# Kernel optimization log

Measured on AMD Instinct MI355X. Metric: run time of the kernel, lower is better.

## Reference

```python
import jax, jax.numpy as jnp
import numpy as np

T, B, D, H = 512, 64, 256, 512


def setup_inputs() -> dict:
    key = jax.random.key(0)
    k1, k2, k3, k4 = jax.random.split(key, 4)
    x = jax.random.normal(k1, (T, B, D), dtype=jnp.float32)
    should_reset = jax.random.randint(k2, (T, B), 0, 2, dtype=jnp.int32)
    # Linear([x, h]) -> 4H gates, Haiku/PyTorch-style fan-in init scale
    scale = 1.0 / np.sqrt(D + H)
    W = jax.random.normal(k3, (D + H, 4 * H), dtype=jnp.float32) * scale
    b = jax.random.normal(k4, (4 * H,), dtype=jnp.float32) * scale
    return {"x": x, "should_reset": should_reset, "W": W, "b": b}


def reference(x, should_reset, W, b):
    """ResetLSTM forward (reverse=False). x:[T,B,D], should_reset:[T,B] -> [T,B,H]."""
    h0 = jnp.zeros((x.shape[1], H), dtype=x.dtype)
    c0 = jnp.zeros((x.shape[1], H), dtype=x.dtype)
    reset = should_reset.astype(x.dtype)[..., None]  # [T,B,1]

    def step(carry, inp):
        h, c = carry
        xt, rt = inp
        keep = 1.0 - rt
        h = h * keep
        c = c * keep
        gates = jnp.concatenate([xt, h], axis=-1) @ W + b  # [B,4H]
        i, g, f, o = jnp.split(gates, 4, axis=-1)
        f = jax.nn.sigmoid(f + 1.0)  # Haiku forget bias +1
        i = jax.nn.sigmoid(i)
        g = jnp.tanh(g)
        o = jax.nn.sigmoid(o)
        new_c = f * c + i * g
        new_h = o * jnp.tanh(new_c)
        return (new_h, new_c), new_h

    _, outputs = jax.lax.scan(step, (h0, c0), (x, reset))
    return outputs  # [T,B,H]
```

## Files before the change

### kernel.cpp

```cpp
#include <hip/hip_runtime.h>

#define TSTEPS 512
#define BATCH  64
#define DIN    256
#define HID    512
#define NCH    8
#define VR     512
#define NRB    16
#define NUB    32
#define NWG    512
#define NTHR   256
#define HSST   520
#define GST    67

typedef __attribute__((ext_vector_type(8))) _Float16 f16x8;
typedef __attribute__((ext_vector_type(4))) _Float16 f16x4;
typedef __attribute__((ext_vector_type(4))) float f32x4;
typedef __attribute__((ext_vector_type(2))) float f32x2;

#define MFMA16(A,B,C) __builtin_amdgcn_mfma_f32_16x16x32_f16(A,B,C,0,0,0)
#define ALDU32(p) __hip_atomic_load(const_cast<unsigned*>(p), __ATOMIC_RELAXED, __HIP_MEMORY_SCOPE_AGENT)
#define ASTU32(p,v) __hip_atomic_store((p), (v), __ATOMIC_RELAXED, __HIP_MEMORY_SCOPE_AGENT)

__device__ __forceinline__ float sigm(float x) { return 1.0f / (1.0f + __expf(-x)); }

__device__ __forceinline__ void gld16_cc(f16x8& d, const void* p) {
  asm volatile("global_load_dwordx4 %0, %1, off sc0 sc1" : "=v"(d) : "v"(p));
}
__device__ __forceinline__ void gld16_l2(f16x8& d, const void* p) {
  asm volatile("global_load_dwordx4 %0, %1, off sc0" : "=v"(d) : "v"(p));
}
__device__ __forceinline__ void gld16_pin(f16x8& d, const void* p) {
  asm volatile("global_load_dwordx4 %0, %1, off" : "=v"(d) : "v"(p));
}

__global__ void conv_x(const float* __restrict__ x, _Float16* __restrict__ xh, int n4) {
  int i = blockIdx.x * 256 + threadIdx.x;
  if (i >= n4) return;
  float4 v = reinterpret_cast<const float4*>(x)[i];
  f16x4 o;
  o[0] = (_Float16)v.x; o[1] = (_Float16)v.y; o[2] = (_Float16)v.z; o[3] = (_Float16)v.w;
  *reinterpret_cast<f16x4*>(xh + (size_t)i * 4) = o;
}

__global__ void w_prep(const float* __restrict__ W,
                       _Float16* __restrict__ WxT, _Float16* __restrict__ WhT) {
  int idx = blockIdx.x * 256 + threadIdx.x;
  if (idx < NUB * 64 * 256) {
    int k = idx & 255, cc = (idx >> 8) & 63, ub = idx >> 14;
    int unit = cc >> 2, g = cc & 3;
    int gcol = g * HID + ub * 16 + unit;
    WxT[idx] = (_Float16)W[k * 2048 + gcol];
  } else if (idx < NUB * 64 * 256 + NUB * 64 * 512) {
    int j = idx - NUB * 64 * 256;
    int k = j & 511, cc = (j >> 9) & 63, ub = j >> 15;
    int unit = cc >> 2, g = cc & 3;
    int gcol = g * HID + ub * 16 + unit;
    WhT[j] = (_Float16)W[(DIN + k) * 2048 + gcol];
  }
}

__global__ void seg_prep(const int* __restrict__ rst, int* __restrict__ tS,
                         int* __restrict__ segLen, int* __restrict__ maxLenB) {
  __shared__ int sMax[NRB];
  const int b = threadIdx.x;
  if (b < NRB) sMax[b] = 0;
  __syncthreads();
  int lo = (TSTEPS + NCH - 1) / NCH, hi = TSTEPS;
  while (lo < hi) {
    int L = (lo + hi) >> 1;
    int pos = 0; bool ok = false;
    for (int s = 0; s < NCH; ++s) {
      int target = pos + L;
      if (target >= TSTEPS) { ok = true; break; }
      int t = target;
      while (t > pos && rst[t * BATCH + b] == 0) --t;
      if (t == pos) break;
      pos = t;
    }
    if (ok) hi = L; else lo = L + 1;
  }
  const int L = lo;
  int pos = 0;
  for (int c = 0; c < NCH; ++c) {
    int start = pos, end = pos;
    if (pos < TSTEPS) {
      int target = pos + L;
      if (target >= TSTEPS) end = TSTEPS;
      else { int t = target; while (t > pos && rst[t * BATCH + b] == 0) --t; end = t; }
      pos = end;
    }
    int vr = c * 64 + b;
    tS[vr] = start;
    segLen[vr] = end - start;
    atomicMax(&sMax[c * 2 + (b >> 5)], end - start);
  }
  __syncthreads();
  if (b < NRB) maxLenB[b] = sMax[b];
}

__global__ void __launch_bounds__(NTHR, 2)
lstm_persistent(const _Float16* __restrict__ xh,
                const int* __restrict__ rst,
                const float* __restrict__ bias,
                float* __restrict__ out,
                unsigned long long* __restrict__ hb,
                unsigned* __restrict__ flags,
                unsigned* __restrict__ xccb,
                const _Float16* __restrict__ WxT,
                const _Float16* __restrict__ WhT,
                const int* __restrict__ tS,
                const int* __restrict__ segLen,
                const int* __restrict__ maxLenB) {
  __shared__ _Float16 hS[32 * HSST];
  __shared__ float gateS[32 * GST];
  __shared__ float biasS[64];
  __shared__ int uniformS;

  const int tid = threadIdx.x, wg = blockIdx.x;
  const int ub = wg >> 4;
  const int rb = ((wg & 7) << 1) | ((wg >> 3) & 1);
  const int wgbase = wg & 15;
  const int vr0 = rb * 32;
  const int lane = tid & 63, wave = tid >> 6;
  const int colA = lane & 15, klo = (lane >> 4) * 8;

  unsigned myxcc;
  asm volatile("s_getreg_b32 %0, hwreg(HW_REG_XCC_ID)" : "=s"(myxcc));
  if (tid == 0) {
    uniformS = 1;
    ASTU32(xccb + wg * 16, 0x100u | (myxcc & 0xffu));
  }
  __syncthreads();
  if (tid < NUB) {
    int mwg = (tid << 4) | wgbase;
    unsigned v;
    do { v = ALDU32(xccb + mwg * 16); if (!v) __builtin_amdgcn_s_sleep(1); } while (!v);
    if ((v & 0xffu) != (myxcc & 0xffu)) uniformS = 0;
  }

  f16x8 wx[8], wh[16];
  {
    const _Float16* px = WxT + ((size_t)ub * 64 + wave * 16 + colA) * 256 + klo;
    const _Float16* ph = WhT + ((size_t)ub * 64 + wave * 16 + colA) * 512 + klo;
#pragma unroll
    for (int ch = 0; ch < 8; ++ch) gld16_pin(wx[ch], px + ch * 32);
#pragma unroll
    for (int ch = 0; ch < 16; ++ch) gld16_pin(wh[ch], ph + ch * 32);
    asm volatile("s_waitcnt vmcnt(0)" ::: "memory");
    __builtin_amdgcn_sched_barrier(0);
  }
  if (tid < 64) {
    int unit = tid >> 2, g = tid & 3;
    biasS[tid] = bias[g * HID + ub * 16 + unit];
  }

  int tSr0 = tS[vr0 + colA];
  int tSr1 = tS[vr0 + 16 + colA];

  const int crow = tid & 31, p = tid >> 5;
  const int vrc = vr0 + crow, bc = vrc & 63;
  const int tSc_ = tS[vrc], lenc_ = segLen[vrc];
  const int ML = maxLenB[rb];
  float cA = 0.f, cB = 0.f;

  __syncthreads();
  const bool useL2 = (uniformS != 0);
  float bA[4], bB[4];
#pragma unroll
  for (int g = 0; g < 4; ++g) { bA[g] = biasS[8 * p + g]; bB[g] = biasS[8 * p + 4 + g]; }

  const int srow = tid >> 3, ss = tid & 7;

  for (int k = 0; k < ML; ++k) {
    f32x4 acc0 = {0.f, 0.f, 0.f, 0.f}, acc1 = {0.f, 0.f, 0.f, 0.f};
    {
      int t0 = tSr0 + k; if (t0 > TSTEPS - 1) t0 = TSTEPS - 1;
      int t1 = tSr1 + k; if (t1 > TSTEPS - 1) t1 = TSTEPS - 1;
      const int b0 = (vr0 + colA) & 63, b1 = (vr0 + 16 + colA) & 63;
      const _Float16* x0 = xh + ((size_t)t0 * BATCH + b0) * DIN + klo;
      const _Float16* x1 = xh + ((size_t)t1 * BATCH + b1) * DIN + klo;
#pragma unroll
      for (int ch = 0; ch < 8; ++ch) {
        f16x8 a0 = *(const f16x8*)(x0 + ch * 32);
        f16x8 a1 = *(const f16x8*)(x1 + ch * 32);
        acc0 = MFMA16(a0, wx[ch], acc0);
        acc1 = MFMA16(a1, wx[ch], acc1);
      }
    }

    if (k) {
      if (tid < NUB) {
        const unsigned tgt = (unsigned)k;
        while (ALDU32(flags + ((tid << 4) | wgbase) * 16) < tgt)
          __builtin_amdgcn_s_sleep(1);
      }
      __syncthreads();
      asm volatile("" ::: "memory");

      {
        const char* hbase = (const char*)hb
            + (((size_t)(k & 1) * (VR * 128) + (size_t)(vr0 + srow) * 128) << 3)
            + ss * 16;
        f16x8 hq[8];
        if (useL2) {
#pragma unroll
          for (int j = 0; j < 8; ++j) gld16_l2(hq[j], hbase + j * 128);
        } else {
#pragma unroll
          for (int j = 0; j < 8; ++j) gld16_cc(hq[j], hbase + j * 128);
        }
        asm volatile("s_waitcnt vmcnt(0)" ::: "memory");
        __builtin_amdgcn_sched_barrier(0);
#pragma unroll
        for (int j = 0; j < 8; ++j)
          *(f16x8*)&hS[srow * HSST + ss * 8 + j * 64] = hq[j];
      }
      __syncthreads();

#pragma unroll
      for (int ch = 0; ch < 16; ++ch) {
        f16x8 a0 = *(const f16x8*)&hS[colA * HSST + ch * 32 + klo];
        f16x8 a1 = *(const f16x8*)&hS[(16 + colA) * HSST + ch * 32 + klo];
        acc0 = MFMA16(a0, wh[ch], acc0);
        acc1 = MFMA16(a1, wh[ch], acc1);
      }
    }

#pragma unroll
    for (int rr = 0; rr < 4; ++rr) {
      int row0 = (lane >> 4) * 4 + rr;
      gateS[row0 * GST + wave * 16 + colA]        = acc0[rr];
      gateS[(16 + row0) * GST + wave * 16 + colA] = acc1[rr];
    }

    float hn0, hn1;
    {
      int kidx = tSc_ + k + 1; if (kidx > TSTEPS - 1) kidx = TSTEPS - 1;
      float keep = 1.0f - (float)rst[kidx * BATCH + bc];
      const float* g = &gateS[crow * GST + 8 * p];
      float i0 = sigm(g[0] + bA[0]);
      float t0 = tanhf(g[1] + bA[1]);
      float f0 = sigm(g[2] + bA[2] + 1.0f);
      float o0 = sigm(g[3] + bA[3]);
      float i1 = sigm(g[4] + bB[0]);
      float t1 = tanhf(g[5] + bB[1]);
      float f1 = sigm(g[6] + bB[2] + 1.0f);
      float o1 = sigm(g[7] + bB[3]);
      float cn0 = f0 * cA + i0 * t0, cn1 = f1 * cB + i1 * t1;
      hn0 = o0 * tanhf(cn0); hn1 = o1 * tanhf(cn1);
      cA = cn0 * keep; cB = cn1 * keep;
      if (k + 1 < ML) {
        union { _Float16 f[2]; unsigned u; } cv;
        cv.f[0] = (_Float16)(hn0 * keep);
        cv.f[1] = (_Float16)(hn1 * keep);
        unsigned* dst = (unsigned*)(hb + (size_t)((k + 1) & 1) * (VR * 128)
                                       + (size_t)vrc * 128) + ub * 8 + p;
        if (useL2)
          asm volatile("global_store_dword %0, %1, off sc0" :: "v"(dst), "v"(cv.u) : "memory");
        else
          ASTU32(dst, cv.u);
      }
    }

    __syncthreads();
    if (k + 1 < ML && tid == 0) ASTU32(flags + wg * 16, (unsigned)(k + 1));

    if (k < lenc_) {
      f32x2 o2 = {hn0, hn1};
      *(f32x2*)&out[((size_t)(tSc_ + k) * BATCH + bc) * HID + ub * 16 + 2 * p] = o2;
    }
  }
}

extern "C" void kernel_launch(void* const* d_in, const int* in_sizes, int n_in,
                              void* d_out, int out_size, void* d_ws, size_t ws_size,
                              hipStream_t stream) {
  const float* x   = (const float*)d_in[0];
  const int*   rst = (const int*)d_in[1];
  const float* W   = (const float*)d_in[2];
  const float* b   = (const float*)d_in[3];
  float* out = (float*)d_out;
  char* ws = (char*)d_ws;

  unsigned*           flags  = (unsigned*)(ws + 0);
  unsigned*           xccb   = (unsigned*)(ws + 32768);
  int*                tSp    = (int*)(ws + 65536);
  int*                segLen = (int*)(ws + 67584);
  int*                maxLenB= (int*)(ws + 69632);
  unsigned long long* hb     = (unsigned long long*)(ws + 73728);
  _Float16*           xh     = (_Float16*)(ws + 73728 + 1048576);
  _Float16*           WxT    = (_Float16*)(ws + 73728 + 1048576 + 16777216);
  _Float16*           WhT    = (_Float16*)(ws + 73728 + 1048576 + 16777216 + 1048576);

  hipMemsetAsync(ws, 0, 65536, stream);

  int n4 = TSTEPS * BATCH * DIN / 4;
  hipLaunchKernelGGL(conv_x, dim3(n4 / 256), dim3(256), 0, stream, x, xh, n4);
  hipLaunchKernelGGL(w_prep, dim3(6144), dim3(256), 0, stream, W, WxT, WhT);
  hipLaunchKernelGGL(seg_prep, dim3(1), dim3(64), 0, stream, rst, tSp, segLen, maxLenB);

  hipLaunchKernelGGL(lstm_persistent, dim3(NWG), dim3(NTHR), 0, stream,
                     xh, rst, b, out, hb, flags, xccb, WxT, WhT, tSp, segLen, maxLenB);
}
```

Measured before the change: 544.7 us.

## Use L2-scoped flag polling/stores and bitmask-based segment cut search

Replaces the per-step flag spin loads and flag stores with sc0 (L2-coherent) loads and stores when the L2 path is enabled, and adds an explicit vmcnt wait before the barrier so that h stores complete before the flag is published. The segment-preparation kernel now builds a per-batch reset bitmask and finds cut points with count-leading-zeros instead of walking backward through global memory. The goal is cheaper inter-workgroup synchronisation and a faster prep kernel. The extra waitcnt adds stall time on each step.

Measured after the change: 576.9 us. 5.9% more time.

```diff
diff --git a/kernel.cpp b/kernel.cpp
--- a/kernel.cpp
+++ b/kernel.cpp
@@ -32,6 +32,15 @@
 }
 __device__ __forceinline__ void gld16_pin(f16x8& d, const void* p) {
   asm volatile("global_load_dwordx4 %0, %1, off" : "=v"(d) : "v"(p));
+}
+__device__ __forceinline__ unsigned fld_l2(const unsigned* p) {
+  unsigned v;
+  asm volatile("global_load_dword %0, %1, off sc0\n\ts_waitcnt vmcnt(0)"
+               : "=v"(v) : "v"(p) : "memory");
+  return v;
+}
+__device__ __forceinline__ void fst_l2(unsigned* p, unsigned v) {
+  asm volatile("global_store_dword %0, %1, off sc0" :: "v"(p), "v"(v) : "memory");
 }
 
 __global__ void conv_x(const float* __restrict__ x, _Float16* __restrict__ xh, int n4) {
@@ -66,6 +75,30 @@
   const int b = threadIdx.x;
   if (b < NRB) sMax[b] = 0;
   __syncthreads();
+
+  unsigned mask[16];
+#pragma unroll
+  for (int w = 0; w < 16; ++w) mask[w] = 0u;
+  for (int t = 1; t < TSTEPS; ++t)
+    if (rst[t * BATCH + b]) mask[t >> 5] |= (1u << (t & 31));
+
+  auto findcut = [&](int pos, int target) -> int {
+    int wHi = target >> 5, wLo = pos >> 5;
+    for (int w = wHi; w >= wLo; --w) {
+      unsigned m = mask[w];
+      if (w == wHi) {
+        int tb = target & 31;
+        if (tb != 31) m &= (1u << (tb + 1)) - 1u;
+      }
+      if (w == wLo) {
+        int pb = pos & 31;
+        m &= (pb == 31) ? 0u : ~((1u << (pb + 1)) - 1u);
+      }
+      if (m) return (w << 5) + (31 - __builtin_clz(m));
+    }
+    return -1;
+  };
+
   int lo = (TSTEPS + NCH - 1) / NCH, hi = TSTEPS;
   while (lo < hi) {
     int L = (lo + hi) >> 1;
@@ -73,10 +106,9 @@
     for (int s = 0; s < NCH; ++s) {
       int target = pos + L;
       if (target >= TSTEPS) { ok = true; break; }
-      int t = target;
-      while (t > pos && rst[t * BATCH + b] == 0) --t;
-      if (t == pos) break;
-      pos = t;
+      int c = findcut(pos, target);
+      if (c < 0) break;
+      pos = c;
     }
     if (ok) hi = L; else lo = L + 1;
   }
@@ -87,7 +119,7 @@
     if (pos < TSTEPS) {
       int target = pos + L;
       if (target >= TSTEPS) end = TSTEPS;
-      else { int t = target; while (t > pos && rst[t * BATCH + b] == 0) --t; end = t; }
+      else { int cc = findcut(pos, target); end = (cc < 0) ? pos : cc; }
       pos = end;
     }
     int vr = c * 64 + b;
@@ -192,8 +224,12 @@
     if (k) {
       if (tid < NUB) {
         const unsigned tgt = (unsigned)k;
-        while (ALDU32(flags + ((tid << 4) | wgbase) * 16) < tgt)
-          __builtin_amdgcn_s_sleep(1);
+        const unsigned* fp = flags + ((tid << 4) | wgbase) * 16;
+        if (useL2) {
+          while (fld_l2(fp) < tgt) __builtin_amdgcn_s_sleep(1);
+        } else {
+          while (ALDU32(fp) < tgt) __builtin_amdgcn_s_sleep(1);
+        }
       }
       __syncthreads();
       asm volatile("" ::: "memory");
@@ -256,15 +292,17 @@
         cv.f[1] = (_Float16)(hn1 * keep);
         unsigned* dst = (unsigned*)(hb + (size_t)((k + 1) & 1) * (VR * 128)
                                        + (size_t)vrc * 128) + ub * 8 + p;
-        if (useL2)
-          asm volatile("global_store_dword %0, %1, off sc0" :: "v"(dst), "v"(cv.u) : "memory");
-        else
-          ASTU32(dst, cv.u);
-      }
-    }
-
+        if (useL2) fst_l2(dst, cv.u);
+        else ASTU32(dst, cv.u);
+      }
+    }
+
+    asm volatile("s_waitcnt vmcnt(0)" ::: "memory");
     __syncthreads();
-    if (k + 1 < ML && tid == 0) ASTU32(flags + wg * 16, (unsigned)(k + 1));
+    if (k + 1 < ML && tid == 0) {
+      if (useL2) fst_l2(flags + wg * 16, (unsigned)(k + 1));
+      else ASTU32(flags + wg * 16, (unsigned)(k + 1));
+    }
 
     if (k < lenc_) {
       f32x2 o2 = {hn0, hn1};
```
